# Kernel tuning notes

Measured on AMD Instinct MI355X. Metric: run time of the kernel, lower is better.

## Reference

```python
import jax, jax.numpy as jnp
from jax import lax
import numpy as np

ARG_NAMES = ('x w1 b1 bn1_g bn1_b bn1_m bn1_v w2 b2 bn2_g bn2_b bn2_m bn2_v w3 b3 w4 b4 '
             'attn_w attn_b attn_u g0_w1 g0_b1 g0_w2 g0_b2 g1_w1 g1_b1 g1_w2 g1_b2 '
             'g2_w1 g2_b1 g2_w2 g2_b2 c_w1 c_b1 c_w2 c_b2 c_w3 c_b3 c_w4 c_b4').split()


def _conv1d(x, w, b, stride, pad):
    # x: [N, C, L], w: [O, I, K]
    y = lax.conv_general_dilated(x, w, (stride,), [(pad, pad)],
                                 dimension_numbers=('NCH', 'OIH', 'NCH'))
    return y + b[None, :, None]


def _bn(x, g, b, m, v, eps=1e-5):
    # eval-mode BatchNorm1d over channel dim of [N, C, L]
    inv = g / jnp.sqrt(v + eps)
    return (x - m[None, :, None]) * inv[None, :, None] + b[None, :, None]


def _forward(x, w1, b1, bn1_g, bn1_b, bn1_m, bn1_v, w2, b2, bn2_g, bn2_b, bn2_m, bn2_v,
             w3, b3, w4, b4, attn_w, attn_b, attn_u,
             g0_w1, g0_b1, g0_w2, g0_b2, g1_w1, g1_b1, g1_w2, g1_b2,
             g2_w1, g2_b1, g2_w2, g2_b2,
             c_w1, c_b1, c_w2, c_b2, c_w3, c_b3, c_w4, c_b4):
    B, S, C, T = x.shape  # [batch, crops, channels=64, time=400]
    h = x.reshape(-1, C, T)
    # CNN stack (dropout = identity in eval)
    h = _bn(jax.nn.elu(_conv1d(h, w1, b1, 2, 1)), bn1_g, bn1_b, bn1_m, bn1_v)   # [N,64,192]
    h = _bn(jax.nn.elu(_conv1d(h, w2, b2, 2, 0)), bn2_g, bn2_b, bn2_m, bn2_v)   # [N,64,87]
    h = jax.nn.elu(_conv1d(h, w3, b3, 1, 0))                                    # [N,64,82]
    h = lax.reduce_window(h, 0.0, lax.add, (1, 1, 3), (1, 1, 2), 'VALID') / 3.0  # [N,64,40]
    h = jax.nn.elu(_conv1d(h, w4, b4, 1, 0))                                    # [N,64,35]
    h = h.reshape(B, S, C, -1)  # [B, S, 64, 35]
    # Attention pooling over the crop dim (dim=1), sum=True
    v = jnp.tanh(jnp.einsum('bsch,hd->bscd', h, attn_w) + attn_b)
    alphas = jax.nn.softmax(jnp.einsum('bscd,d->bsc', v, attn_u), axis=1)
    h = jax.nn.elu((h * alphas[..., None]).sum(axis=1))  # [B, 64, 35]
    # GIN over complete 64-node graph (self-loops included, eps=0):
    # aggregation per node == sum over all nodes of the graph
    def gin(h, W1, B1, W2, B2):
        agg = h + h.sum(axis=1, keepdims=True)
        return jax.nn.relu(agg @ W1 + B1) @ W2 + B2
    h = jax.nn.relu(gin(h, g0_w1, g0_b1, g0_w2, g0_b2))
    h = jax.nn.relu(gin(h, g1_w1, g1_b1, g1_w2, g1_b2))
    h = gin(h, g2_w1, g2_b1, g2_w2, g2_b2)  # no act after last layer
    # Classifier
    f = h.reshape(B, -1)  # [B, 2240]
    f = jax.nn.elu(f @ c_w1 + c_b1)
    f = jax.nn.elu(f @ c_w2 + c_b2)
    f = jax.nn.elu(f @ c_w3 + c_b3)
    return f @ c_w4 + c_b4  # [B, 2]


def setup_inputs() -> dict:
    key = jax.random.key(0)
    ks = iter(jax.random.split(key, 64))
    def rn(shape, s=0.05):
        return jax.random.normal(next(ks), shape, dtype=jnp.float32) * s
    d = {}
    d['x'] = jax.random.normal(next(ks), (32, 16, 64, 400), dtype=jnp.float32)
    d['w1'] = rn((64, 64, 20)); d['b1'] = rn((64,))
    d['bn1_g'] = jnp.ones((64,), jnp.float32); d['bn1_b'] = jnp.zeros((64,), jnp.float32)
    d['bn1_m'] = jnp.zeros((64,), jnp.float32); d['bn1_v'] = jnp.ones((64,), jnp.float32)
    d['w2'] = rn((64, 64, 20)); d['b2'] = rn((64,))
    d['bn2_g'] = jnp.ones((64,), jnp.float32); d['bn2_b'] = jnp.zeros((64,), jnp.float32)
    d['bn2_m'] = jnp.zeros((64,), jnp.float32); d['bn2_v'] = jnp.ones((64,), jnp.float32)
    d['w3'] = rn((64, 64, 6)); d['b3'] = rn((64,))
    d['w4'] = rn((64, 64, 6)); d['b4'] = rn((64,))
    d['attn_w'] = rn((35, 256), 0.1); d['attn_b'] = rn((256,), 0.1); d['attn_u'] = rn((256,), 0.1)
    d['g0_w1'] = rn((35, 256)); d['g0_b1'] = rn((256,))
    d['g0_w2'] = rn((256, 256)); d['g0_b2'] = rn((256,))
    d['g1_w1'] = rn((256, 256)); d['g1_b1'] = rn((256,))
    d['g1_w2'] = rn((256, 256)); d['g1_b2'] = rn((256,))
    d['g2_w1'] = rn((256, 35)); d['g2_b1'] = rn((35,))
    d['g2_w2'] = rn((35, 35)); d['g2_b2'] = rn((35,))
    d['c_w1'] = rn((2240, 256)); d['c_b1'] = rn((256,))
    d['c_w2'] = rn((256, 64)); d['c_b2'] = rn((64,))
    d['c_w3'] = rn((64, 16)); d['c_b3'] = rn((16,))
    d['c_w4'] = rn((16, 2)); d['c_b4'] = rn((2,))
    return d


def reference(x, w1, b1, bn1_g, bn1_b, bn1_m, bn1_v, w2, b2, bn2_g, bn2_b, bn2_m, bn2_v,
              w3, b3, w4, b4, attn_w, attn_b, attn_u,
              g0_w1, g0_b1, g0_w2, g0_b2, g1_w1, g1_b1, g1_w2, g1_b2,
              g2_w1, g2_b1, g2_w2, g2_b2,
              c_w1, c_b1, c_w2, c_b2, c_w3, c_b3, c_w4, c_b4):
    return _forward(x, w1, b1, bn1_g, bn1_b, bn1_m, bn1_v, w2, b2, bn2_g, bn2_b, bn2_m, bn2_v,
                    w3, b3, w4, b4, attn_w, attn_b, attn_u,
                    g0_w1, g0_b1, g0_w2, g0_b2, g1_w1, g1_b1, g1_w2, g1_b2,
                    g2_w1, g2_b1, g2_w2, g2_b2,
                    c_w1, c_b1, c_w2, c_b2, c_w3, c_b3, c_w4, c_b4)
```

## Files before the change

kernel.cpp:

```cpp
#include <hip/hip_runtime.h>
#include <math.h>

typedef __attribute__((ext_vector_type(8))) __bf16 bf16x8;
typedef __attribute__((ext_vector_type(4))) float f32x4;

__device__ __forceinline__ float elu_f(float v) {
    return v > 0.f ? v : (expf(v) - 1.f);
}

__global__ __launch_bounds__(256) void prep_weights(
    const float* __restrict__ w1, const float* __restrict__ w2,
    const float* __restrict__ w3, const float* __restrict__ w4,
    __bf16* __restrict__ t1, __bf16* __restrict__ t2,
    __bf16* __restrict__ t3, __bf16* __restrict__ t4)
{
    int idx = blockIdx.x * 256 + threadIdx.x;
    if (idx < 81920) {
        int k = idx / 4096, r = idx - k * 4096, co = r >> 6, ci = r & 63;
        t1[idx] = (__bf16)w1[(co * 64 + ci) * 20 + k];
    } else if (idx < 163840) {
        int j = idx - 81920;
        int k = j / 4096, r = j - k * 4096, co = r >> 6, ci = r & 63;
        t2[j] = (__bf16)w2[(co * 64 + ci) * 20 + k];
    } else if (idx < 188416) {
        int j = idx - 163840;
        int k = j / 4096, r = j - k * 4096, co = r >> 6, ci = r & 63;
        t3[j] = (__bf16)w3[(co * 64 + ci) * 6 + k];
    } else if (idx < 212992) {
        int j = idx - 188416;
        int k = j / 4096, r = j - k * 4096, co = r >> 6, ci = r & 63;
        t4[j] = (__bf16)w4[(co * 64 + ci) * 6 + k];
    }
}

__global__ __launch_bounds__(256) void prep_tr(
    const float* __restrict__ g0w1, const float* __restrict__ g0w2,
    const float* __restrict__ g1w1, const float* __restrict__ g1w2,
    const float* __restrict__ g2w1, const float* __restrict__ g2w2,
    __bf16* __restrict__ d0, __bf16* __restrict__ d1, __bf16* __restrict__ d2,
    __bf16* __restrict__ d3, __bf16* __restrict__ d4, __bf16* __restrict__ d5)
{
    int bid = blockIdx.x;
    const float* src; __bf16* dst; int K, O, Kpad, Opad, tile;
    if (bid < 4)       { src = g0w1; dst = d0; K = 35;   O = 256; Kpad = 64;   Opad = 256; tile = bid; }
    else if (bid < 20) { src = g0w2; dst = d1; K = 256;  O = 256; Kpad = 256;  Opad = 256; tile = bid - 4; }
    else if (bid < 36) { src = g1w1; dst = d2; K = 256;  O = 256; Kpad = 256;  Opad = 256; tile = bid - 20; }
    else if (bid < 52) { src = g1w2; dst = d3; K = 256;  O = 256; Kpad = 256;  Opad = 256; tile = bid - 36; }
    else if (bid < 56) { src = g2w1; dst = d4; K = 256;  O = 35;  Kpad = 256;  Opad = 64;  tile = bid - 52; }
    else               { src = g2w2; dst = d5; K = 35;   O = 35;  Kpad = 64;   Opad = 64;  tile = 0; }
    int ktiles = Kpad >> 6;
    int ot = tile / ktiles, kt = tile - ot * ktiles;
    int k0 = kt * 64, o0 = ot * 64;
    size_t LOFF = (size_t)Opad * Kpad;
    __shared__ float tl[64][68];
    int c = threadIdx.x & 63, rr = threadIdx.x >> 6;
    #pragma unroll
    for (int it = 0; it < 16; ++it) {
        int r = rr + it * 4;
        int kk = k0 + r, oo = o0 + c;
        tl[r][c] = (kk < K && oo < O) ? src[(size_t)kk * O + oo] : 0.f;
    }
    __syncthreads();
    #pragma unroll
    for (int it = 0; it < 16; ++it) {
        int r = rr + it * 4;
        float v = tl[c][r];
        __bf16 hi = (__bf16)v;
        float lo = v - (float)hi;
        size_t pos = (size_t)(o0 + r) * Kpad + k0 + c;
        dst[pos] = hi;
        dst[LOFF + pos] = (__bf16)lo;
    }
}

template<int K, int STRIDE, int PAD, bool DO_BN, int IMODE,
         int NPB, int TPN, int LIN, int LOUT, int KCHUNK>
__global__ __launch_bounds__(NPB * TPN * 64, 2) void conv_mfma(
    const void* __restrict__ xin, const __bf16* __restrict__ wT,
    const float* __restrict__ bias,
    const float* __restrict__ bn_g, const float* __restrict__ bn_b,
    const float* __restrict__ bn_m, const float* __restrict__ bn_v,
    __bf16* __restrict__ y)
{
    constexpr int THREADS = NPB * TPN * 64;
    constexpr int TBLK  = TPN * 48;
    constexpr int VSPAN = STRIDE * (TBLK - 1) + K;
    constexpr int NBUF  = (STRIDE == 2) ? 2 : 1;
    constexpr int ROWS  = (VSPAN + NBUF - 1) / NBUF;
    __shared__ __align__(16) __bf16 sx[NPB * NBUF * ROWS * 72];
    __shared__ __align__(16) __bf16 sw[KCHUNK * 64 * 72];

    const int tid = threadIdx.x;
    const int nb  = blockIdx.x * NPB;

    if constexpr (IMODE == 0) {
        const float* xg = (const float*)xin + (size_t)nb * 64 * LIN;
        constexpr int NZROWS = PAD + (VSPAN - LIN - PAD);
        if (tid < NZROWS * 64) {
            int zr = tid >> 6;
            int v = (zr < PAD) ? zr : (LIN + PAD + zr - PAD);
            sx[((v & (NBUF - 1)) * ROWS + (v >> (NBUF - 1))) * 72 + (tid & 63)] = (__bf16)0.f;
        }
        constexpr int J4 = LIN / 4;
        constexpr int NCH = 64 * J4;
        constexpr int ITER = NCH / THREADS;
        #pragma unroll
        for (int it = 0; it < ITER; ++it) {
            int idx = it * THREADS + tid;
            int ci = idx / J4, j = idx - ci * J4;
            float4 f = *(const float4*)(xg + (size_t)ci * LIN + 4 * j);
            #pragma unroll
            for (int e = 0; e < 4; ++e) {
                int v = 4 * j + e + PAD;
                sx[((v & (NBUF - 1)) * ROWS + (v >> (NBUF - 1))) * 72 + ci] =
                    (__bf16)((e == 0) ? f.x : (e == 1) ? f.y : (e == 2) ? f.z : f.w);
            }
        }
    }

    const int wave = tid >> 6, lane = tid & 63;
    const int n_l  = wave / TPN, tile = wave - n_l * TPN;
    const int m    = lane & 15, quad = lane >> 4;
    const __bf16* sxn = sx + (size_t)n_l * NBUF * ROWS * 72;

    f32x4 acc[3][4];
    #pragma unroll
    for (int mi = 0; mi < 3; ++mi)
        #pragma unroll
        for (int nj = 0; nj < 4; ++nj)
            acc[mi][nj] = (f32x4){0.f, 0.f, 0.f, 0.f};

    for (int kb = 0; kb < K; kb += KCHUNK) {
        if (kb) __syncthreads();
        constexpr int WITER = KCHUNK * 64 * 8 / THREADS;
        #pragma unroll
        for (int it = 0; it < WITER; ++it) {
            int idx = it * THREADS + tid;
            int r = idx >> 3, p = idx & 7;
            *(uint4*)(sw + (size_t)r * 72 + p * 8) =
                *(const uint4*)(wT + (size_t)(kb + (r >> 6)) * 4096 + (r & 63) * 64 + p * 8);
        }
        __syncthreads();

        #pragma unroll
        for (int kp2 = 0; kp2 < KCHUNK; ++kp2) {
            const int kp = kb + kp2;
            const int buf    = (STRIDE == 2) ? (kp & 1) : 0;
            const int rowoff = (STRIDE == 2) ? (kp >> 1) : kp;
            const __bf16* abase = sxn + ((size_t)buf * ROWS + tile * 48 + m + rowoff) * 72;
            const __bf16* bbase = sw + (size_t)(kp2 * 64 + m) * 72;
            #pragma unroll
            for (int s = 0; s < 2; ++s) {
                bf16x8 af[3], bfr[4];
                #pragma unroll
                for (int mi = 0; mi < 3; ++mi)
                    af[mi] = *(const bf16x8*)(abase + mi * (16 * 72) + s * 32 + quad * 8);
                #pragma unroll
                for (int nj = 0; nj < 4; ++nj)
                    bfr[nj] = *(const bf16x8*)(bbase + nj * (16 * 72) + s * 32 + quad * 8);
                #pragma unroll
                for (int mi = 0; mi < 3; ++mi)
                    #pragma unroll
                    for (int nj = 0; nj < 4; ++nj)
                        acc[mi][nj] = __builtin_amdgcn_mfma_f32_16x16x32_bf16(
                            af[mi], bfr[nj], acc[mi][nj], 0, 0, 0);
            }
        }
    }

    #pragma unroll
    for (int nj = 0; nj < 4; ++nj) {
        const int co = nj * 16 + m;
        const float bi = bias[co];
        float scale = 1.f, shift = 0.f;
        if constexpr (DO_BN) {
            float inv = bn_g[co] / sqrtf(bn_v[co] + 1e-5f);
            scale = inv; shift = bn_b[co] - bn_m[co] * inv;
        }
        #pragma unroll
        for (int mi = 0; mi < 3; ++mi) {
            #pragma unroll
            for (int r = 0; r < 4; ++r) {
                int t = tile * 48 + mi * 16 + quad * 4 + r;
                if (t < LOUT) {
                    float v = acc[mi][nj][r] + bi;
                    v = elu_f(v);
                    if constexpr (DO_BN) v = v * scale + shift;
                    y[((size_t)(nb + n_l) * LOUT + t) * 64 + co] = (__bf16)v;
                }
            }
        }
    }
}

__global__ __launch_bounds__(128, 2) void conv234_fused(
    const __bf16* __restrict__ h1,
    const __bf16* __restrict__ wT2, const float* __restrict__ b2,
    const float* __restrict__ bn2g, const float* __restrict__ bn2b,
    const float* __restrict__ bn2m, const float* __restrict__ bn2v,
    const __bf16* __restrict__ wT3, const float* __restrict__ b3,
    const __bf16* __restrict__ wT4, const float* __restrict__ b4,
    __bf16* __restrict__ h4)
{
    __shared__ __align__(16) __bf16 bufA[2 * 96 * 72];
    __shared__ __align__(16) __bf16 bufB[87 * 72];
    __shared__ __align__(16) __bf16 sw[2 * 64 * 72];

    const int tid = threadIdx.x;
    const int n = blockIdx.x;
    const int wave = tid >> 6, lane = tid & 63;
    const int m = lane & 15, quad = lane >> 4;

    {
        const __bf16* src = h1 + (size_t)n * 192 * 64;
        #pragma unroll
        for (int it = 0; it < 12; ++it) {
            int idx = it * 128 + tid;
            int v = idx >> 3, c8 = (idx & 7) * 8;
            *(uint4*)(bufA + ((size_t)(v & 1) * 96 + (v >> 1)) * 72 + c8) =
                *(const uint4*)(src + (size_t)v * 64 + c8);
        }
    }
    __syncthreads();

    f32x4 acc[3][4];
    #pragma unroll
    for (int mi = 0; mi < 3; ++mi)
        #pragma unroll
        for (int nj = 0; nj < 4; ++nj)
            acc[mi][nj] = (f32x4){0.f, 0.f, 0.f, 0.f};

    for (int kb = 0; kb < 20; kb += 2) {
        if (kb) __syncthreads();
        #pragma unroll
        for (int it = 0; it < 8; ++it) {
            int idx = it * 128 + tid;
            int r = idx >> 3, p = idx & 7;
            *(uint4*)(sw + (size_t)r * 72 + p * 8) =
                *(const uint4*)(wT2 + (size_t)(kb + (r >> 6)) * 4096 + (r & 63) * 64 + p * 8);
        }
        __syncthreads();
        #pragma unroll
        for (int kp2 = 0; kp2 < 2; ++kp2) {
            const int kp = kb + kp2;
            const int buf = kp & 1, rowoff = kp >> 1;
            const int r0 = wave * 48 + m + rowoff;
            const __bf16* bbase = sw + (size_t)(kp2 * 64 + m) * 72;
            #pragma unroll
            for (int s = 0; s < 2; ++s) {
                bf16x8 af[3], bfr[4];
                #pragma unroll
                for (int mi = 0; mi < 3; ++mi) {
                    int rr = r0 + mi * 16; if (rr > 95) rr = 95;
                    af[mi] = *(const bf16x8*)(bufA + ((size_t)buf * 96 + rr) * 72 + s * 32 + quad * 8);
                }
                #pragma unroll
                for (int nj = 0; nj < 4; ++nj)
                    bfr[nj] = *(const bf16x8*)(bbase + nj * (16 * 72) + s * 32 + quad * 8);
                #pragma unroll
                for (int mi = 0; mi < 3; ++mi)
                    #pragma unroll
                    for (int nj = 0; nj < 4; ++nj)
                        acc[mi][nj] = __builtin_amdgcn_mfma_f32_16x16x32_bf16(
                            af[mi], bfr[nj], acc[mi][nj], 0, 0, 0);
            }
        }
    }
    __syncthreads();
    #pragma unroll
    for (int nj = 0; nj < 4; ++nj) {
        const int co = nj * 16 + m;
        const float bi = b2[co];
        float inv = bn2g[co] / sqrtf(bn2v[co] + 1e-5f);
        float shift = bn2b[co] - bn2m[co] * inv;
        #pragma unroll
        for (int mi = 0; mi < 3; ++mi)
            #pragma unroll
            for (int r = 0; r < 4; ++r) {
                int t = wave * 48 + mi * 16 + quad * 4 + r;
                if (t < 87) {
                    float v = elu_f(acc[mi][nj][r] + bi) * inv + shift;
                    bufB[t * 72 + co] = (__bf16)v;
                }
            }
    }
    __syncthreads();

    #pragma unroll
    for (int mi = 0; mi < 3; ++mi)
        #pragma unroll
        for (int nj = 0; nj < 4; ++nj)
            acc[mi][nj] = (f32x4){0.f, 0.f, 0.f, 0.f};

    for (int kb = 0; kb < 6; kb += 2) {
        if (kb) __syncthreads();
        #pragma unroll
        for (int it = 0; it < 8; ++it) {
            int idx = it * 128 + tid;
            int r = idx >> 3, p = idx & 7;
            *(uint4*)(sw + (size_t)r * 72 + p * 8) =
                *(const uint4*)(wT3 + (size_t)(kb + (r >> 6)) * 4096 + (r & 63) * 64 + p * 8);
        }
        __syncthreads();
        #pragma unroll
        for (int kp2 = 0; kp2 < 2; ++kp2) {
            const int kp = kb + kp2;
            const int r0 = wave * 48 + m + kp;
            const __bf16* bbase = sw + (size_t)(kp2 * 64 + m) * 72;
            #pragma unroll
            for (int s = 0; s < 2; ++s) {
                bf16x8 af[3], bfr[4];
                #pragma unroll
                for (int mi = 0; mi < 3; ++mi) {
                    int rr = r0 + mi * 16; if (rr > 86) rr = 86;
                    af[mi] = *(const bf16x8*)(bufB + (size_t)rr * 72 + s * 32 + quad * 8);
                }
                #pragma unroll
                for (int nj = 0; nj < 4; ++nj)
                    bfr[nj] = *(const bf16x8*)(bbase + nj * (16 * 72) + s * 32 + quad * 8);
                #pragma unroll
                for (int mi = 0; mi < 3; ++mi)
                    #pragma unroll
                    for (int nj = 0; nj < 4; ++nj)
                        acc[mi][nj] = __builtin_amdgcn_mfma_f32_16x16x32_bf16(
                            af[mi], bfr[nj], acc[mi][nj], 0, 0, 0);
            }
        }
    }
    __syncthreads();
    #pragma unroll
    for (int nj = 0; nj < 4; ++nj) {
        const int co = nj * 16 + m;
        const float bi = b3[co];
        #pragma unroll
        for (int mi = 0; mi < 3; ++mi)
            #pragma unroll
            for (int r = 0; r < 4; ++r) {
                int t = wave * 48 + mi * 16 + quad * 4 + r;
                if (t < 82)
                    bufA[t * 72 + co] = (__bf16)elu_f(acc[mi][nj][r] + bi);
            }
    }
    __syncthreads();

    #pragma unroll
    for (int it = 0; it < 20; ++it) {
        int idx = it * 128 + tid;
        int t = idx >> 6, co = idx & 63;
        float v = ((float)bufA[(2 * t) * 72 + co] + (float)bufA[(2 * t + 1) * 72 + co] +
                   (float)bufA[(2 * t + 2) * 72 + co]) * (1.f / 3.f);
        bufB[t * 72 + co] = (__bf16)v;
    }
    __syncthreads();

    f32x4 acc4[3][2];
    #pragma unroll
    for (int mi = 0; mi < 3; ++mi)
        #pragma unroll
        for (int nj = 0; nj < 2; ++nj)
            acc4[mi][nj] = (f32x4){0.f, 0.f, 0.f, 0.f};
    const int coh = wave * 32;

    for (int kb = 0; kb < 6; kb += 2) {
        if (kb) __syncthreads();
        #pragma unroll
        for (int it = 0; it < 8; ++it) {
            int idx = it * 128 + tid;
            int r = idx >> 3, p = idx & 7;
            *(uint4*)(sw + (size_t)r * 72 + p * 8) =
                *(const uint4*)(wT4 + (size_t)(kb + (r >> 6)) * 4096 + (r & 63) * 64 + p * 8);
        }
        __syncthreads();
        #pragma unroll
        for (int kp2 = 0; kp2 < 2; ++kp2) {
            const int kp = kb + kp2;
            const int r0 = m + kp;
            const __bf16* bbase = sw + (size_t)(kp2 * 64 + coh + m) * 72;
            #pragma unroll
            for (int s = 0; s < 2; ++s) {
                bf16x8 af[3], bfr[2];
                #pragma unroll
                for (int mi = 0; mi < 3; ++mi) {
                    int rr = r0 + mi * 16; if (rr > 39) rr = 39;
                    af[mi] = *(const bf16x8*)(bufB + (size_t)rr * 72 + s * 32 + quad * 8);
                }
                #pragma unroll
                for (int nj = 0; nj < 2; ++nj)
                    bfr[nj] = *(const bf16x8*)(bbase + nj * (16 * 72) + s * 32 + quad * 8);
                #pragma unroll
                for (int mi = 0; mi < 3; ++mi)
                    #pragma unroll
                    for (int nj = 0; nj < 2; ++nj)
                        acc4[mi][nj] = __builtin_amdgcn_mfma_f32_16x16x32_bf16(
                            af[mi], bfr[nj], acc4[mi][nj], 0, 0, 0);
            }
        }
    }
    #pragma unroll
    for (int nj = 0; nj < 2; ++nj) {
        const int co = coh + nj * 16 + m;
        const float bi = b4[co];
        #pragma unroll
        for (int mi = 0; mi < 3; ++mi)
            #pragma unroll
            for (int r = 0; r < 4; ++r) {
                int t = mi * 16 + quad * 4 + r;
                if (t < 35)
                    h4[((size_t)n * 35 + t) * 64 + co] = (__bf16)elu_f(acc4[mi][nj][r] + bi);
            }
    }
}

__global__ __launch_bounds__(256) void attn_pool_k(
    const __bf16* __restrict__ h, const float* __restrict__ W,
    const float* __restrict__ ab, const float* __restrict__ u,
    float* __restrict__ out)
{
    __shared__ float sW[35 * 256];
    __shared__ float sh[4][16 * 35 + 5];
    const int tid = threadIdx.x;
    const int pair0 = blockIdx.x * 4;
    for (int i = tid; i < 35 * 256; i += 256) sW[i] = W[i];
    for (int i = tid; i < 4 * 560; i += 256) {
        int q = i / 560, r = i - q * 560;
        int s = r / 35, t = r - s * 35;
        int bc = pair0 + q, b = bc >> 6, c = bc & 63;
        sh[q][s * 35 + t] = (float)h[(((size_t)b * 16 + s) * 35 + t) * 64 + c];
    }
    __syncthreads();

    const int wave = tid >> 6, lane = tid & 63;
    const int bc = pair0 + wave;
    const float* shw = sh[wave];

    float myu[4], myb[4];
    #pragma unroll
    for (int p = 0; p < 4; ++p) { myu[p] = u[lane + 64 * p]; myb[p] = ab[lane + 64 * p]; }

    float dot[16][4];
    #pragma unroll
    for (int s = 0; s < 16; ++s)
        #pragma unroll
        for (int p = 0; p < 4; ++p) dot[s][p] = myb[p];

    for (int t = 0; t < 35; ++t) {
        float w0 = sW[t * 256 + lane];
        float w1 = sW[t * 256 + lane + 64];
        float w2 = sW[t * 256 + lane + 128];
        float w3 = sW[t * 256 + lane + 192];
        #pragma unroll
        for (int s = 0; s < 16; ++s) {
            float hv = shw[s * 35 + t];
            dot[s][0] = fmaf(hv, w0, dot[s][0]);
            dot[s][1] = fmaf(hv, w1, dot[s][1]);
            dot[s][2] = fmaf(hv, w2, dot[s][2]);
            dot[s][3] = fmaf(hv, w3, dot[s][3]);
        }
    }

    float sc[16];
    #pragma unroll
    for (int s = 0; s < 16; ++s) {
        float v = tanhf(dot[s][0]) * myu[0] + tanhf(dot[s][1]) * myu[1]
                + tanhf(dot[s][2]) * myu[2] + tanhf(dot[s][3]) * myu[3];
        #pragma unroll
        for (int off = 1; off < 64; off <<= 1) v += __shfl_xor(v, off, 64);
        sc[s] = v;
    }

    float mx = sc[0];
    #pragma unroll
    for (int s = 1; s < 16; ++s) mx = fmaxf(mx, sc[s]);
    float e[16], sum = 0.f;
    #pragma unroll
    for (int s = 0; s < 16; ++s) { e[s] = expf(sc[s] - mx); sum += e[s]; }
    float inv = 1.f / sum;

    if (lane < 35) {
        float acc = 0.f;
        #pragma unroll
        for (int s = 0; s < 16; ++s) acc = fmaf(shw[s * 35 + lane], e[s] * inv, acc);
        out[(size_t)bc * 35 + lane] = elu_f(acc);
    }
}

#define APLANE (64 * 264)

__device__ __forceinline__ void gin_gemm_dev(
    const __bf16* As,
    const __bf16* __restrict__ Wg, int Kpad, int wlo, int Kout,
    const float* __restrict__ bias,
    int mode, __bf16* Ad, float* __restrict__ outg)
{
    const int lane = threadIdx.x & 63;
    const int wave = threadIdx.x >> 6;
    const int o0 = wave * 32;
    if (o0 >= ((Kout + 63) & ~63)) return;
    const int m = lane & 15, quad = lane >> 4;

    f32x4 acc[4][2];
    #pragma unroll
    for (int mi = 0; mi < 4; ++mi)
        #pragma unroll
        for (int nj = 0; nj < 2; ++nj)
            acc[mi][nj] = (f32x4){0.f, 0.f, 0.f, 0.f};

    for (int k0 = 0; k0 < Kpad; k0 += 32) {
        bf16x8 ah[4], al[4], bh[2], bl[2];
        #pragma unroll
        for (int mi = 0; mi < 4; ++mi) {
            const __bf16* ap = As + (size_t)(mi * 16 + m) * 264 + k0 + quad * 8;
            ah[mi] = *(const bf16x8*)ap;
            al[mi] = *(const bf16x8*)(ap + APLANE);
        }
        #pragma unroll
        for (int nj = 0; nj < 2; ++nj) {
            const __bf16* wp = Wg + (size_t)(o0 + nj * 16 + m) * Kpad + k0 + quad * 8;
            bh[nj] = *(const bf16x8*)wp;
            bl[nj] = *(const bf16x8*)(wp + wlo);
        }
        #pragma unroll
        for (int mi = 0; mi < 4; ++mi)
            #pragma unroll
            for (int nj = 0; nj < 2; ++nj) {
                acc[mi][nj] = __builtin_amdgcn_mfma_f32_16x16x32_bf16(
                    al[mi], bh[nj], acc[mi][nj], 0, 0, 0);
                acc[mi][nj] = __builtin_amdgcn_mfma_f32_16x16x32_bf16(
                    ah[mi], bl[nj], acc[mi][nj], 0, 0, 0);
                acc[mi][nj] = __builtin_amdgcn_mfma_f32_16x16x32_bf16(
                    ah[mi], bh[nj], acc[mi][nj], 0, 0, 0);
            }
    }

    #pragma unroll
    for (int nj = 0; nj < 2; ++nj) {
        const int o = o0 + nj * 16 + m;
        const bool ovalid = (o < Kout);
        const float bi = ovalid ? bias[o] : 0.f;
        float v[4][4];
        #pragma unroll
        for (int mi = 0; mi < 4; ++mi)
            #pragma unroll
            for (int r = 0; r < 4; ++r)
                v[mi][r] = acc[mi][nj][r] + bi;
        if (mode == 2) {
            if (ovalid) {
                #pragma unroll
                for (int mi = 0; mi < 4; ++mi)
                    #pragma unroll
                    for (int r = 0; r < 4; ++r)
                        outg[(size_t)(mi * 16 + quad * 4 + r) * Kout + o] = v[mi][r];
            }
        } else {
            float s = 0.f;
            #pragma unroll
            for (int mi = 0; mi < 4; ++mi)
                #pragma unroll
                for (int r = 0; r < 4; ++r) {
                    float rv = ovalid ? fmaxf(v[mi][r], 0.f) : 0.f;
                    v[mi][r] = rv;
                    s += rv;
                }
            if (mode == 1) {
                s += __shfl_xor(s, 16, 64);
                s += __shfl_xor(s, 32, 64);
            } else {
                s = 0.f;
            }
            #pragma unroll
            for (int mi = 0; mi < 4; ++mi)
                #pragma unroll
                for (int r = 0; r < 4; ++r) {
                    float a = v[mi][r] + s;
                    __bf16 hi = (__bf16)a;
                    size_t pos = (size_t)(mi * 16 + quad * 4 + r) * 264 + o;
                    Ad[pos] = hi;
                    Ad[APLANE + pos] = (__bf16)(a - (float)hi);
                }
        }
    }
}

__global__ __launch_bounds__(512) void gin_fused(
    const float* __restrict__ ha,
    const __bf16* __restrict__ gW0a, const __bf16* __restrict__ gW0b,
    const __bf16* __restrict__ gW1a, const __bf16* __restrict__ gW1b,
    const __bf16* __restrict__ gW2a, const __bf16* __restrict__ gW2b,
    const float* __restrict__ b0a, const float* __restrict__ b0b,
    const float* __restrict__ b1a, const float* __restrict__ b1b,
    const float* __restrict__ b2a, const float* __restrict__ b2b,
    float* __restrict__ H3)
{
    const int b = blockIdx.x, tid = threadIdx.x;
    __shared__ __align__(16) __bf16 sA[2][2 * APLANE];
    __shared__ float sS[64];
    const float* hab = ha + (size_t)b * 2240;

    if (tid < 64) {
        float s = 0.f;
        if (tid < 35)
            for (int n = 0; n < 64; ++n) s += hab[n * 35 + tid];
        sS[tid] = s;
    }
    __syncthreads();
    for (int idx = tid; idx < 64 * 64; idx += 512) {
        int n = idx >> 6, k = idx & 63;
        float a = (k < 35) ? hab[n * 35 + k] + sS[k] : 0.f;
        __bf16 hi = (__bf16)a;
        sA[0][n * 264 + k] = hi;
        sA[0][APLANE + n * 264 + k] = (__bf16)(a - (float)hi);
    }
    __syncthreads();

    gin_gemm_dev(sA[0], gW0a, 64,  16384, 256, b0a, 0, sA[1], nullptr); __syncthreads();
    gin_gemm_dev(sA[1], gW0b, 256, 65536, 256, b0b, 1, sA[0], nullptr); __syncthreads();
    gin_gemm_dev(sA[0], gW1a, 256, 65536, 256, b1a, 0, sA[1], nullptr); __syncthreads();
    gin_gemm_dev(sA[1], gW1b, 256, 65536, 256, b1b, 1, sA[0], nullptr); __syncthreads();
    gin_gemm_dev(sA[0], gW2a, 256, 16384, 35,  b2a, 0, sA[1], nullptr); __syncthreads();
    gin_gemm_dev(sA[1], gW2b, 64,  4096,  35,  b2b, 2, nullptr, H3 + (size_t)b * 2240);
}

__global__ __launch_bounds__(256) void cls1_part_k(
    const float* __restrict__ H3, const float* __restrict__ w1,
    float* __restrict__ s1p)
{
    const int b  = blockIdx.x;
    const int kc = blockIdx.y;
    const int k0 = kc * 140;
    __shared__ float sH[140];
    const int tid = threadIdx.x;
    if (tid < 140) sH[tid] = H3[(size_t)b * 2240 + k0 + tid];
    __syncthreads();
    const int o = (tid >> 6) * 64 + (tid & 63);
    float a0 = 0.f, a1 = 0.f, a2 = 0.f, a3 = 0.f;
    const float* wr = w1 + (size_t)k0 * 256 + o;
    #pragma unroll
    for (int k = 0; k < 140; k += 4) {
        a0 = fmaf(sH[k],     wr[(size_t)k * 256],       a0);
        a1 = fmaf(sH[k + 1], wr[(size_t)(k + 1) * 256], a1);
        a2 = fmaf(sH[k + 2], wr[(size_t)(k + 2) * 256], a2);
        a3 = fmaf(sH[k + 3], wr[(size_t)(k + 3) * 256], a3);
    }
    s1p[((size_t)kc * 32 + b) * 256 + o] = a0 + a1 + a2 + a3;
}

__global__ __launch_bounds__(256) void cls234_k(
    const float* __restrict__ s1p, const float* __restrict__ b1,
    const float* __restrict__ w2, const float* __restrict__ b2,
    const float* __restrict__ w3, const float* __restrict__ b3,
    const float* __restrict__ w4, const float* __restrict__ b4,
    float* __restrict__ out)
{
    const int b = blockIdx.x, tid = threadIdx.x;
    __shared__ float s1[256];
    __shared__ float part[4][64];
    __shared__ float s2[64];
    __shared__ float s3[16];
    {
        float acc = b1[tid];
        #pragma unroll
        for (int kc = 0; kc < 16; ++kc)
            acc += s1p[((size_t)kc * 32 + b) * 256 + tid];
        s1[tid] = elu_f(acc);
    }
    __syncthreads();
    {
        int kg = tid >> 6, o = tid & 63;
        float acc = 0.f;
        for (int k = kg * 64; k < kg * 64 + 64; ++k)
            acc = fmaf(s1[k], w2[k * 64 + o], acc);
        part[kg][o] = acc;
    }
    __syncthreads();
    if (tid < 64) {
        float acc = part[0][tid] + part[1][tid] + part[2][tid] + part[3][tid] + b2[tid];
        s2[tid] = elu_f(acc);
    }
    __syncthreads();
    if (tid < 16) {
        float acc = b3[tid];
        for (int k = 0; k < 64; ++k) acc = fmaf(s2[k], w3[k * 16 + tid], acc);
        s3[tid] = elu_f(acc);
    }
    __syncthreads();
    if (tid < 2) {
        float acc = b4[tid];
        for (int k = 0; k < 16; ++k) acc = fmaf(s3[k], w4[k * 2 + tid], acc);
        out[b * 2 + tid] = acc;
    }
}

extern "C" void kernel_launch(void* const* d_in, const int* in_sizes, int n_in,
                              void* d_out, int out_size, void* d_ws, size_t ws_size,
                              hipStream_t stream)
{
    const float* x     = (const float*)d_in[0];
    const float* w1    = (const float*)d_in[1];
    const float* b1    = (const float*)d_in[2];
    const float* bn1_g = (const float*)d_in[3];
    const float* bn1_b = (const float*)d_in[4];
    const float* bn1_m = (const float*)d_in[5];
    const float* bn1_v = (const float*)d_in[6];
    const float* w2    = (const float*)d_in[7];
    const float* b2    = (const float*)d_in[8];
    const float* bn2_g = (const float*)d_in[9];
    const float* bn2_b = (const float*)d_in[10];
    const float* bn2_m = (const float*)d_in[11];
    const float* bn2_v = (const float*)d_in[12];
    const float* w3    = (const float*)d_in[13];
    const float* b3    = (const float*)d_in[14];
    const float* w4    = (const float*)d_in[15];
    const float* b4    = (const float*)d_in[16];
    const float* attn_w = (const float*)d_in[17];
    const float* attn_b = (const float*)d_in[18];
    const float* attn_u = (const float*)d_in[19];
    const float* g0_w1 = (const float*)d_in[20];
    const float* g0_b1 = (const float*)d_in[21];
    const float* g0_w2 = (const float*)d_in[22];
    const float* g0_b2 = (const float*)d_in[23];
    const float* g1_w1 = (const float*)d_in[24];
    const float* g1_b1 = (const float*)d_in[25];
    const float* g1_w2 = (const float*)d_in[26];
    const float* g1_b2 = (const float*)d_in[27];
    const float* g2_w1 = (const float*)d_in[28];
    const float* g2_b1 = (const float*)d_in[29];
    const float* g2_w2 = (const float*)d_in[30];
    const float* g2_b2 = (const float*)d_in[31];
    const float* c_w1  = (const float*)d_in[32];
    const float* c_b1  = (const float*)d_in[33];
    const float* c_w2  = (const float*)d_in[34];
    const float* c_b2  = (const float*)d_in[35];
    const float* c_w3  = (const float*)d_in[36];
    const float* c_b3  = (const float*)d_in[37];
    const float* c_w4  = (const float*)d_in[38];
    const float* c_b4  = (const float*)d_in[39];
    float* out = (float*)d_out;

    char* ws = (char*)d_ws;
    __bf16* wT1  = (__bf16*)(ws + 0);
    __bf16* wT2  = (__bf16*)(ws + 163840);
    __bf16* wT3  = (__bf16*)(ws + 327680);
    __bf16* wT4  = (__bf16*)(ws + 376832);
    __bf16* h1   = (__bf16*)(ws + 425984);
    __bf16* h4   = (__bf16*)(ws + 13008896);
    float*  ha   = (float*)(ws + 15302656);
    __bf16* gW0a = (__bf16*)(ws + 15589376);
    __bf16* gW0b = (__bf16*)(ws + 15654912);
    __bf16* gW1a = (__bf16*)(ws + 15917056);
    __bf16* gW1b = (__bf16*)(ws + 16179200);
    __bf16* gW2a = (__bf16*)(ws + 16441344);
    __bf16* gW2b = (__bf16*)(ws + 16506880);
    float*  H3   = (float*)(ws + 16523264);
    float*  s1p  = (float*)(ws + 16809984);

    prep_weights<<<dim3(832), dim3(256), 0, stream>>>(w1, w2, w3, w4, wT1, wT2, wT3, wT4);
    prep_tr<<<dim3(57), dim3(256), 0, stream>>>(g0_w1, g0_w2, g1_w1, g1_w2, g2_w1, g2_w2,
                                                gW0a, gW0b, gW1a, gW1b, gW2a, gW2b);

    conv_mfma<20, 2, 1, true, 0, 1, 4, 400, 192, 2><<<dim3(512), dim3(256), 0, stream>>>(
        x, wT1, b1, bn1_g, bn1_b, bn1_m, bn1_v, h1);

    conv234_fused<<<dim3(512), dim3(128), 0, stream>>>(
        h1, wT2, b2, bn2_g, bn2_b, bn2_m, bn2_v, wT3, b3, wT4, b4, h4);

    attn_pool_k<<<dim3(512), dim3(256), 0, stream>>>(h4, attn_w, attn_b, attn_u, ha);

    gin_fused<<<dim3(32), dim3(512), 0, stream>>>(
        ha, gW0a, gW0b, gW1a, gW1b, gW2a, gW2b,
        g0_b1, g0_b2, g1_b1, g1_b2, g2_b1, g2_b2, H3);

    cls1_part_k<<<dim3(32, 16), dim3(256), 0, stream>>>(H3, c_w1, s1p);
    cls234_k<<<dim3(32), dim3(256), 0, stream>>>(s1p, c_b1, c_w2, c_b2, c_w3, c_b3,
                                                 c_w4, c_b4, out);
}
```

Before: 308.3 us.

## Double-buffer conv weight taps via registers and vectorize input transpose loads

Replaces the chunked weight staging (KCHUNK taps per barrier) with a per-tap double buffer in LDS: the next tap's weights are prefetched into registers during the current tap's MFMA work, then written to the alternate buffer before a single barrier. The fp32 input load now reads 4x4 blocks so each thread writes packed bf16x4 vectors to LDS instead of scalar bf16 stores. This is meant to hide global weight latency and cut LDS store count, at the cost of one barrier per tap and more registers.

```diff
diff --git a/kernel.cpp b/kernel.cpp
--- a/kernel.cpp
+++ b/kernel.cpp
@@ -2,6 +2,7 @@
 #include <math.h>
 
 typedef __attribute__((ext_vector_type(8))) __bf16 bf16x8;
+typedef __attribute__((ext_vector_type(4))) __bf16 bf16x4;
 typedef __attribute__((ext_vector_type(4))) float f32x4;
 
 __device__ __forceinline__ float elu_f(float v) {
@@ -74,7 +75,7 @@
 }
 
 template<int K, int STRIDE, int PAD, bool DO_BN, int IMODE,
-         int NPB, int TPN, int LIN, int LOUT, int KCHUNK>
+         int NPB, int TPN, int LIN, int LOUT, int KCHUNK >
 __global__ __launch_bounds__(NPB * TPN * 64, 2) void conv_mfma(
     const void* __restrict__ xin, const __bf16* __restrict__ wT,
     const float* __restrict__ bias,
@@ -88,7 +89,7 @@
     constexpr int NBUF  = (STRIDE == 2) ? 2 : 1;
     constexpr int ROWS  = (VSPAN + NBUF - 1) / NBUF;
     __shared__ __align__(16) __bf16 sx[NPB * NBUF * ROWS * 72];
-    __shared__ __align__(16) __bf16 sw[KCHUNK * 64 * 72];
+    __shared__ __align__(16) __bf16 sw[2 * 64 * 72];
 
     const int tid = threadIdx.x;
     const int nb  = blockIdx.x * NPB;
@@ -102,18 +103,27 @@
             sx[((v & (NBUF - 1)) * ROWS + (v >> (NBUF - 1))) * 72 + (tid & 63)] = (__bf16)0.f;
         }
         constexpr int J4 = LIN / 4;
-        constexpr int NCH = 64 * J4;
-        constexpr int ITER = NCH / THREADS;
+        constexpr int ITEMS = 16 * J4;
+        constexpr int ITER = (ITEMS + THREADS - 1) / THREADS;
         #pragma unroll
         for (int it = 0; it < ITER; ++it) {
             int idx = it * THREADS + tid;
-            int ci = idx / J4, j = idx - ci * J4;
-            float4 f = *(const float4*)(xg + (size_t)ci * LIN + 4 * j);
-            #pragma unroll
-            for (int e = 0; e < 4; ++e) {
-                int v = 4 * j + e + PAD;
-                sx[((v & (NBUF - 1)) * ROWS + (v >> (NBUF - 1))) * 72 + ci] =
-                    (__bf16)((e == 0) ? f.x : (e == 1) ? f.y : (e == 2) ? f.z : f.w);
+            if (ITEMS % THREADS == 0 || idx < ITEMS) {
+                int jj = idx & 3;
+                int g  = (idx >> 2) & 15;
+                int q  = (idx >> 6) * 4 + jj;
+                const float* xp = xg + (size_t)(4 * g) * LIN + 4 * q;
+                float fa[4][4];
+                #pragma unroll
+                for (int u = 0; u < 4; ++u)
+                    *(float4*)&fa[u][0] = *(const float4*)(xp + (size_t)u * LIN);
+                #pragma unroll
+                for (int e = 0; e < 4; ++e) {
+                    int v = 4 * q + e + PAD;
+                    bf16x4 wv = { (__bf16)fa[0][e], (__bf16)fa[1][e],
+                                  (__bf16)fa[2][e], (__bf16)fa[3][e] };
+                    *(bf16x4*)&sx[((v & (NBUF - 1)) * ROWS + (v >> (NBUF - 1))) * 72 + 4 * g] = wv;
+                }
             }
         }
     }
@@ -130,42 +140,58 @@
         for (int nj = 0; nj < 4; ++nj)
             acc[mi][nj] = (f32x4){0.f, 0.f, 0.f, 0.f};
 
-    for (int kb = 0; kb < K; kb += KCHUNK) {
-        if (kb) __syncthreads();
-        constexpr int WITER = KCHUNK * 64 * 8 / THREADS;
-        #pragma unroll
-        for (int it = 0; it < WITER; ++it) {
-            int idx = it * THREADS + tid;
-            int r = idx >> 3, p = idx & 7;
-            *(uint4*)(sw + (size_t)r * 72 + p * 8) =
-                *(const uint4*)(wT + (size_t)(kb + (r >> 6)) * 4096 + (r & 63) * 64 + p * 8);
+    constexpr int WPT = (64 * 8) / THREADS;
+    uint4 wreg[WPT];
+    #pragma unroll
+    for (int i = 0; i < WPT; ++i) {
+        int idx = i * THREADS + tid;
+        wreg[i] = *(const uint4*)(wT + (size_t)(idx >> 3) * 64 + (idx & 7) * 8);
+    }
+    #pragma unroll
+    for (int i = 0; i < WPT; ++i) {
+        int idx = i * THREADS + tid;
+        *(uint4*)(sw + (size_t)(idx >> 3) * 72 + (idx & 7) * 8) = wreg[i];
+    }
+    __syncthreads();
+
+    for (int kp = 0; kp < K; ++kp) {
+        if (kp + 1 < K) {
+            #pragma unroll
+            for (int i = 0; i < WPT; ++i) {
+                int idx = i * THREADS + tid;
+                wreg[i] = *(const uint4*)(wT + (size_t)(kp + 1) * 4096 +
+                                          (idx >> 3) * 64 + (idx & 7) * 8);
+            }
+        }
+        const int xbuf   = (STRIDE == 2) ? (kp & 1) : 0;
+        const int rowoff = (STRIDE == 2) ? (kp >> 1) : kp;
+        const __bf16* abase = sxn + ((size_t)xbuf * ROWS + tile * 48 + m + rowoff) * 72;
+        const __bf16* bbase = sw + (size_t)((kp & 1) * 64 + m) * 72;
+        #pragma unroll
+        for (int s = 0; s < 2; ++s) {
+            bf16x8 af[3], bfr[4];
+            #pragma unroll
+            for (int mi = 0; mi < 3; ++mi)
+                af[mi] = *(const bf16x8*)(abase + mi * (16 * 72) + s * 32 + quad * 8);
+            #pragma unroll
+            for (int nj = 0; nj < 4; ++nj)
+                bfr[nj] = *(const bf16x8*)(bbase + nj * (16 * 72) + s * 32 + quad * 8);
+            #pragma unroll
+            for (int mi = 0; mi < 3; ++mi)
+                #pragma unroll
+                for (int nj = 0; nj < 4; ++nj)
+                    acc[mi][nj] = __builtin_amdgcn_mfma_f32_16x16x32_bf16(
+                        af[mi], bfr[nj], acc[mi][nj], 0, 0, 0);
+        }
+        if (kp + 1 < K) {
+            __bf16* swd = sw + (size_t)((kp + 1) & 1) * 64 * 72;
+            #pragma unroll
+            for (int i = 0; i < WPT; ++i) {
+                int idx = i * THREADS + tid;
+                *(uint4*)(swd + (size_t)(idx >> 3) * 72 + (idx & 7) * 8) = wreg[i];
+            }
         }
         __syncthreads();
-
-        #pragma unroll
-        for (int kp2 = 0; kp2 < KCHUNK; ++kp2) {
-            const int kp = kb + kp2;
-            const int buf    = (STRIDE == 2) ? (kp & 1) : 0;
-            const int rowoff = (STRIDE == 2) ? (kp >> 1) : kp;
-            const __bf16* abase = sxn + ((size_t)buf * ROWS + tile * 48 + m + rowoff) * 72;
-            const __bf16* bbase = sw + (size_t)(kp2 * 64 + m) * 72;
-            #pragma unroll
-            for (int s = 0; s < 2; ++s) {
-                bf16x8 af[3], bfr[4];
-                #pragma unroll
-                for (int mi = 0; mi < 3; ++mi)
-                    af[mi] = *(const bf16x8*)(abase + mi * (16 * 72) + s * 32 + quad * 8);
-                #pragma unroll
-                for (int nj = 0; nj < 4; ++nj)
-                    bfr[nj] = *(const bf16x8*)(bbase + nj * (16 * 72) + s * 32 + quad * 8);
-                #pragma unroll
-                for (int mi = 0; mi < 3; ++mi)
-                    #pragma unroll
-                    for (int nj = 0; nj < 4; ++nj)
-                        acc[mi][nj] = __builtin_amdgcn_mfma_f32_16x16x32_bf16(
-                            af[mi], bfr[nj], acc[mi][nj], 0, 0, 0);
-            }
-        }
     }
 
     #pragma unroll
```

After: 304.0 us. Within noise of the previous version (-1.4%).
